# Kernel tuning notes

Measured on AMD Instinct MI355X. Metric: run time of the kernel, lower is better.

The kernel has to match this reference:

```python
import jax, jax.numpy as jnp
import numpy as np

B, F, U, H1, H2 = 2048, 256, 64, 64, 32
E = F + 1  # attention embed dim = num_inputs + 1


def setup_inputs() -> dict:
    key = jax.random.key(0)
    ks = jax.random.split(key, 14)
    s = lambda fan: 1.0 / np.sqrt(fan)
    inp = {
        "x": jax.random.normal(ks[0], (B, F), jnp.float32),
        # stacked per-feature FeatureNN params (Linear(1,U) -> Linear(U,H1) -> Linear(H1,H2) -> Linear(H2,1))
        "w1": jax.random.normal(ks[1], (F, U), jnp.float32) * s(1),
        "b1": jnp.zeros((F, U), jnp.float32),
        "w2": jax.random.normal(ks[2], (F, U, H1), jnp.float32) * s(U),
        "b2": jnp.zeros((F, H1), jnp.float32),
        "w3": jax.random.normal(ks[3], (F, H1, H2), jnp.float32) * s(H1),
        "b3": jnp.zeros((F, H2), jnp.float32),
        "w4": jax.random.normal(ks[4], (F, H2), jnp.float32) * s(H2),
        "b4": jnp.zeros((F,), jnp.float32),
        # MultiheadAttention(E, 1) params: packed qkv in_proj + out_proj
        "in_w": jax.random.normal(ks[5], (3 * E, E), jnp.float32) * s(E),
        "in_b": jnp.zeros((3 * E,), jnp.float32),
        "out_w": jax.random.normal(ks[6], (E, E), jnp.float32) * s(E),
        "out_b": jnp.zeros((E,), jnp.float32),
        "bias": jnp.zeros((1,), jnp.float32),
    }
    return inp


def _attention(x, in_w, in_b, out_w, out_b):
    # x: [B, F]; build [B, F, E] = concat(one-hot feature index, value)
    b = x.shape[0]
    eye = jnp.eye(F, dtype=x.dtype)
    xa = jnp.concatenate([jnp.broadcast_to(eye, (b, F, F)), x[:, :, None]], axis=-1)  # [B,F,E]
    qkv = jnp.einsum("bse,fe->bsf", xa, in_w) + in_b  # [B,F,3E]
    q, k, v = jnp.split(qkv, 3, axis=-1)
    scores = jnp.einsum("bqe,bke->bqk", q, k) / jnp.sqrt(jnp.asarray(E, x.dtype))
    attn = jax.nn.softmax(scores, axis=-1)
    ctx = jnp.einsum("bqk,bke->bqe", attn, v)
    out = jnp.einsum("bqe,fe->bqf", ctx, out_w) + out_b  # out_proj
    return out[:, :, -1]  # keep only the value channel -> [B, F]


def _feature_nns(x, w1, b1, w2, b2, w3, b3, w4, b4):
    # x: [B, F] -> per-feature independent MLPs, batched across features
    h = jax.nn.relu(x[:, :, None] * w1[None] + b1[None])          # [B,F,U]
    h = jax.nn.relu(jnp.einsum("bfu,fuh->bfh", h, w2) + b2[None])  # [B,F,H1]
    h = jax.nn.relu(jnp.einsum("bfh,fhg->bfg", h, w3) + b3[None])  # [B,F,H2]
    return jnp.einsum("bfg,fg->bf", h, w4) + b4[None]              # [B,F]


def reference(x, w1, b1, w2, b2, w3, b3, w4, b4, in_w, in_b, out_w, out_b, bias):
    xa = _attention(x, in_w, in_b, out_w, out_b)                   # att_before_flag=True
    fo = _feature_nns(xa, w1, b1, w2, b2, w3, b3, w4, b4)          # dropout is identity (p=0 / eval)
    out = jnp.sum(fo, axis=-1) + bias                              # [B] + bias -> [B]
    return (out, fo)
```

## Files before the change

### kernel.cpp

```cpp
#include <hip/hip_runtime.h>

#define BB 2048
#define FF 256
#define EE 257
#define UU 64
#define HH1 64
#define HH2 32

#define SC 0.089992807f

typedef __attribute__((ext_vector_type(8))) short short8;
typedef __attribute__((ext_vector_type(4))) float f32x4;
typedef __attribute__((ext_vector_type(4))) unsigned u32x4;
typedef __attribute__((ext_vector_type(2))) unsigned u32x2;

#define MF(a, b, c) __builtin_amdgcn_mfma_f32_16x16x32_bf16(a, b, c, 0, 0, 0)
#define EXP2(x) __builtin_amdgcn_exp2f(x)

__device__ inline unsigned cvt_pk(float a, float b) {
    unsigned r;
    asm("v_cvt_pk_bf16_f32 %0, %1, %2" : "=v"(r) : "v"(a), "v"(b));
    return r;
}
struct HiLo { unsigned hi, lo; };
__device__ inline HiLo split2(float a, float b) {
    HiLo r;
    r.hi = cvt_pk(a, b);
    float ha = __builtin_bit_cast(float, r.hi << 16);
    float hb = __builtin_bit_cast(float, r.hi & 0xFFFF0000u);
    r.lo = cvt_pk(a - ha, b - hb);
    return r;
}
__device__ inline f32x4 splat4(float v) { f32x4 r; r[0]=v; r[1]=v; r[2]=v; r[3]=v; return r; }

__global__ __launch_bounds__(256) void k_prep(const float* __restrict__ in_w,
                                              const float* __restrict__ in_b,
                                              const float* __restrict__ out_w,
                                              const float* __restrict__ out_b,
                                              const float* __restrict__ w2,
                                              const float* __restrict__ w3,
                                              float* __restrict__ mt,
                                              float* __restrict__ uv, float* __restrict__ wgf,
                                              float* __restrict__ sc,
                                              short* __restrict__ w2s, short* __restrict__ w3s) {
    const int blk = blockIdx.x;
    const int t = threadIdx.x;
    __shared__ float red[4][256];
    __shared__ float s0[EE + 3];
    __shared__ float s1[EE + 3];
    if (blk < 256) {
        const int ki = blk;
        for (int j = t; j < EE; j += 256) {
            s0[j] = in_w[(EE + j) * EE + ki] + in_b[EE + j];
            s1[j] = in_b[j];
        }
        __syncthreads();
        const int w = t >> 6, l = t & 63;
        const int j0 = (w * EE) >> 2, j1 = ((w + 1) * EE) >> 2;
        float acc[4] = {0.f, 0.f, 0.f, 0.f};
#pragma unroll 4
        for (int j = j0; j < j1; ++j) {
            float ak = s0[j];
            float bj = s1[j];
#pragma unroll
            for (int g = 0; g < 4; ++g) {
                float aq = in_w[j * EE + l + 64 * g] + bj;
                acc[g] = fmaf(aq, ak, acc[g]);
            }
        }
#pragma unroll
        for (int g = 0; g < 4; ++g) red[w][l + 64 * g] = acc[g];
        __syncthreads();
        {
            float s = red[0][t] + red[1][t] + red[2][t] + red[3][t];
            mt[(ki >> 1) * 512 + t * 2 + (ki & 1)] = s * SC;
        }
    } else if (blk < 512) {
        const int f = blk - 256;
        const int l = t & 63, q = t >> 6;
        const int lr = l & 15, lq = l >> 4;
        const float* w2f = w2 + f * (UU * HH1);
        const float* w3f = w3 + f * (HH1 * HH2);
        short* o2 = w2s + f * 8192;
        short* o3 = w3s + f * 4096;
#pragma unroll
        for (int kb = 0; kb < 2; ++kb) {
            float v[8];
#pragma unroll
            for (int j = 0; j < 8; ++j) v[j] = w2f[(kb * 32 + lq * 8 + j) * HH1 + q * 16 + lr];
            u32x4 hi, lo;
#pragma unroll
            for (int p = 0; p < 4; ++p) {
                HiLo s = split2(v[2 * p], v[2 * p + 1]);
                hi[p] = s.hi; lo[p] = s.lo;
            }
            *(short8*)(o2 + ((0 * 2 + kb) * 4 + q) * 512 + l * 8) = __builtin_bit_cast(short8, hi);
            *(short8*)(o2 + ((1 * 2 + kb) * 4 + q) * 512 + l * 8) = __builtin_bit_cast(short8, lo);
        }
        {
            const int kb = q & 1, ct = q >> 1;
            float v[8];
#pragma unroll
            for (int j = 0; j < 8; ++j) v[j] = w3f[(kb * 32 + lq * 8 + j) * HH2 + ct * 16 + lr];
            u32x4 hi, lo;
#pragma unroll
            for (int p = 0; p < 4; ++p) {
                HiLo s = split2(v[2 * p], v[2 * p + 1]);
                hi[p] = s.hi; lo[p] = s.lo;
            }
            *(short8*)(o3 + ((0 * 2 + kb) * 2 + ct) * 512 + l * 8) = __builtin_bit_cast(short8, hi);
            *(short8*)(o3 + ((1 * 2 + kb) * 2 + ct) * 512 + l * 8) = __builtin_bit_cast(short8, lo);
        }
    } else if (blk < 515) {
        const int which = blk - 512;
        for (int j = t; j < EE; j += 256) {
            if (which == 0)      { s0[j] = in_w[(EE + j) * EE + FF];    s1[j] = in_b[j]; }
            else if (which == 1) { s0[j] = in_w[j * EE + FF];           s1[j] = in_b[EE + j]; }
            else                 { s0[j] = out_w[(EE - 1) * EE + j];    s1[j] = in_b[2 * EE + j]; }
        }
        __syncthreads();
        const int w = t >> 6, l = t & 63;
        const int j0 = (w * EE) >> 2, j1 = ((w + 1) * EE) >> 2;
        const int rowbase = which * EE;
        float acc[4] = {0.f, 0.f, 0.f, 0.f};
#pragma unroll 4
        for (int j = j0; j < j1; ++j) {
            float sk = s0[j];
            float bj = s1[j];
#pragma unroll
            for (int g = 0; g < 4; ++g) {
                float av = in_w[(rowbase + j) * EE + l + 64 * g] + bj;
                acc[g] = fmaf(av, sk, acc[g]);
            }
        }
#pragma unroll
        for (int g = 0; g < 4; ++g) red[w][l + 64 * g] = acc[g];
        __syncthreads();
        {
            float s = red[0][t] + red[1][t] + red[2][t] + red[3][t];
            if (which == 0)      uv[t]          = s * SC;
            else if (which == 1) wgf[2 * t]     = s * SC;
            else                 wgf[2 * t + 1] = s;
        }
    } else {
        const int j = t;
        float cq = in_w[j * EE + FF];
        float ck = in_w[(EE + j) * EE + FF];
        float cv = in_w[(2 * EE + j) * EE + FF];
        float rj = out_w[(EE - 1) * EE + j];
        float pa = cq * ck, pb = cv * rj;
        if (t == 0) {
            const int j2 = 256;
            pa += in_w[j2 * EE + FF] * in_w[(EE + j2) * EE + FF];
            pb += in_w[(2 * EE + j2) * EE + FF] * out_w[(EE - 1) * EE + j2];
        }
#pragma unroll
        for (int o = 32; o > 0; o >>= 1) {
            pa += __shfl_down(pa, o, 64);
            pb += __shfl_down(pb, o, 64);
        }
        if ((t & 63) == 0) { red[0][t >> 6] = pa; red[1][t >> 6] = pb; }
        __syncthreads();
        if (t == 0) {
            pa = red[0][0] + red[0][1] + red[0][2] + red[0][3];
            pb = red[1][0] + red[1][1] + red[1][2] + red[1][3];
            sc[0] = pa * SC;
            sc[1] = pb;
            sc[2] = out_b[EE - 1];
        }
    }
}

__global__ __launch_bounds__(256) void k2_attn(const float* __restrict__ x,
                                               const float2* __restrict__ mt2,
                                               const float* __restrict__ uv,
                                               const float* __restrict__ wg,
                                               const float* __restrict__ sc,
                                               float* __restrict__ xa) {
    const int qi = threadIdx.x;
    const int b0 = blockIdx.x * 2;
    __shared__ __align__(16) float xs0[FF];
    __shared__ __align__(16) float xs1[FF];
    __shared__ __align__(16) float wgs[2 * FF];
    xs0[qi] = x[b0 * FF + qi];
    xs1[qi] = x[(b0 + 1) * FF + qi];
    *(float2*)&wgs[2 * qi] = *(const float2*)&wg[2 * qi];
    const float alpha_s = sc[0], beta = sc[1], ob = sc[2];
    const float uq = uv[qi];
    __syncthreads();
    const float xq0 = xs0[qi];
    const float xq1 = xs1[qi];
    const float a0 = fmaf(alpha_s, xq0, uq);
    const float a1 = fmaf(alpha_s, xq1, uq);
    float le0 = 0.f, le1 = 0.f, p0 = 0.f, p1 = 0.f, q0 = 0.f, q1 = 0.f;
#pragma unroll 8
    for (int kp = 0; kp < FF / 2; ++kp) {
        const float2 m   = mt2[kp * FF + qi];
        const f32x4 wgk  = *(const f32x4*)&wgs[4 * kp];
        const float2 xk0 = *(const float2*)&xs0[2 * kp];
        const float2 xk1 = *(const float2*)&xs1[2 * kp];
        float e;
        e = EXP2(fmaf(xk0.x, a0, fmaf(wgk[0], xq0, m.x))); le0 += e; p0 = fmaf(e, wgk[1], p0); q0 = fmaf(e, xk0.x, q0);
        e = EXP2(fmaf(xk0.y, a0, fmaf(wgk[2], xq0, m.y))); le0 += e; p0 = fmaf(e, wgk[3], p0); q0 = fmaf(e, xk0.y, q0);
        e = EXP2(fmaf(xk1.x, a1, fmaf(wgk[0], xq1, m.x))); le1 += e; p1 = fmaf(e, wgk[1], p1); q1 = fmaf(e, xk1.x, q1);
        e = EXP2(fmaf(xk1.y, a1, fmaf(wgk[2], xq1, m.y))); le1 += e; p1 = fmaf(e, wgk[3], p1); q1 = fmaf(e, xk1.y, q1);
    }
    xa[b0 * FF + qi]       = (p0 + beta * q0) / le0 + ob;
    xa[(b0 + 1) * FF + qi] = (p1 + beta * q1) / le1 + ob;
}

__global__ __launch_bounds__(256, 3) void k3_fnn(const float* xa_in,
                                                 const float* __restrict__ w1,
                                                 const float* __restrict__ b1,
                                                 const float* __restrict__ b2,
                                                 const float* __restrict__ b3,
                                                 const float* __restrict__ w4,
                                                 const float* __restrict__ b4,
                                                 const short* __restrict__ w2s,
                                                 const short* __restrict__ w3s,
                                                 float* fo) {
    const int f   = blockIdx.x & 255;
    const int rq  = blockIdx.x >> 8;
    const int tid = threadIdx.x;
    const int wv  = tid >> 6;
    const int l   = tid & 63;
    const int lr  = l & 15;
    const int lq  = l >> 4;

    const float* w1f = w1 + f * UU;
    const float* b1f = b1 + f * UU;
    const float* b2f = b2 + f * HH1;
    const float* b3f = b3 + f * HH2;
    const float* w4f = w4 + f * HH2;
    const short* w2sf = w2s + f * 8192;
    const short* w3sf = w3s + f * 4096;

    const float B3s0 = b3f[lr], B3s1 = b3f[16 + lr];
    const float w4v0 = w4f[lr], w4v1 = w4f[16 + lr];
    const float b4v  = b4[f];

    short8 W3h[2][2], W3l[2][2];
#pragma unroll
    for (int ct = 0; ct < 2; ++ct)
#pragma unroll
        for (int kb = 0; kb < 2; ++kb) {
            W3h[ct][kb] = *(const short8*)(w3sf + ((0 * 2 + kb) * 2 + ct) * 512 + l * 8);
            W3l[ct][kb] = *(const short8*)(w3sf + ((1 * 2 + kb) * 2 + ct) * 512 + l * 8);
        }

    __shared__ __align__(16) short w2l[8192];
#pragma unroll
    for (int i = 0; i < 4; ++i)
        *(short8*)(w2l + (tid * 4 + i) * 8) = *(const short8*)(w2sf + (tid * 4 + i) * 8);

    __shared__ __align__(16) short lds2[4][32][2][64];
    short* myl = &lds2[wv][0][0][0];

    __syncthreads();

    const int cstart = (rq * 64) / 3;
    const int cend   = ((rq + 1) * 64) / 3;
    for (int ch = cstart + wv; ch < cend; ch += 4) {
        const int rows0 = ch * 32;

        const float xv0 = xa_in[(rows0 + lr) * FF + f];
        const float xv1 = xa_in[(rows0 + 16 + lr) * FF + f];
        short8 Bh[2][2], Bl[2][2];
#pragma unroll
        for (int kb = 0; kb < 2; ++kb) {
            f32x4 wA = *(const f32x4*)(w1f + kb * 32 + lq * 8);
            f32x4 wB = *(const f32x4*)(w1f + kb * 32 + lq * 8 + 4);
            f32x4 bA = *(const f32x4*)(b1f + kb * 32 + lq * 8);
            f32x4 bB = *(const f32x4*)(b1f + kb * 32 + lq * 8 + 4);
#pragma unroll
            for (int rbt = 0; rbt < 2; ++rbt) {
                const float xv = rbt ? xv1 : xv0;
                float h[8];
#pragma unroll
                for (int j = 0; j < 4; ++j) h[j]     = fmaxf(fmaf(xv, wA[j], bA[j]), 0.f);
#pragma unroll
                for (int j = 0; j < 4; ++j) h[4 + j] = fmaxf(fmaf(xv, wB[j], bB[j]), 0.f);
                u32x4 bh, bl;
#pragma unroll
                for (int p = 0; p < 4; ++p) {
                    HiLo s = split2(h[2 * p], h[2 * p + 1]);
                    bh[p] = s.hi; bl[p] = s.lo;
                }
                Bh[rbt][kb] = __builtin_bit_cast(short8, bh);
                Bl[rbt][kb] = __builtin_bit_cast(short8, bl);
            }
        }

#pragma unroll
        for (int ht = 0; ht < 4; ++ht) {
            const short8 W2h0 = *(const short8*)(w2l + (0 * 4 + ht) * 512 + l * 8);
            const short8 W2h1 = *(const short8*)(w2l + (1 * 4 + ht) * 512 + l * 8);
            const short8 W2l0 = *(const short8*)(w2l + (2 * 4 + ht) * 512 + l * 8);
            const short8 W2l1 = *(const short8*)(w2l + (3 * 4 + ht) * 512 + l * 8);
            const f32x4 binit = *(const f32x4*)(b2f + ht * 16 + lq * 4);
#pragma unroll
            for (int rbt = 0; rbt < 2; ++rbt) {
                f32x4 acc = binit;
                acc = MF(W2h0, Bh[rbt][0], acc);
                acc = MF(W2h1, Bh[rbt][1], acc);
                acc = MF(W2h0, Bl[rbt][0], acc);
                acc = MF(W2h1, Bl[rbt][1], acc);
                acc = MF(W2l0, Bh[rbt][0], acc);
                acc = MF(W2l1, Bh[rbt][1], acc);
                const int row = rbt * 16 + lr;
                const int swz = (row & 7) << 3;
                const int hb  = (ht * 16 + lq * 4) ^ swz;
                float v0 = fmaxf(acc[0], 0.f), v1 = fmaxf(acc[1], 0.f);
                float v2 = fmaxf(acc[2], 0.f), v3 = fmaxf(acc[3], 0.f);
                HiLo p0 = split2(v0, v1);
                HiLo p1 = split2(v2, v3);
                u32x2 hiw, low;
                hiw[0] = p0.hi; hiw[1] = p1.hi;
                low[0] = p0.lo; low[1] = p1.lo;
                *(u32x2*)(myl + row * 128 + hb)      = hiw;
                *(u32x2*)(myl + row * 128 + 64 + hb) = low;
            }
        }

#pragma unroll
        for (int rbt = 0; rbt < 2; ++rbt) {
            const int row = rbt * 16 + lr;
            const int swz = (row & 7) << 3;
            const short8 Ah0 = *(const short8*)(myl + row * 128 + ((0  + lq * 8) ^ swz));
            const short8 Ah1 = *(const short8*)(myl + row * 128 + ((32 + lq * 8) ^ swz));
            const short8 Al0 = *(const short8*)(myl + row * 128 + 64 + ((0  + lq * 8) ^ swz));
            const short8 Al1 = *(const short8*)(myl + row * 128 + 64 + ((32 + lq * 8) ^ swz));
            f32x4 a0 = splat4(B3s0);
            f32x4 a1 = splat4(B3s1);
            a0 = MF(Ah0, W3h[0][0], a0); a0 = MF(Ah1, W3h[0][1], a0);
            a0 = MF(Ah0, W3l[0][0], a0); a0 = MF(Ah1, W3l[0][1], a0);
            a0 = MF(Al0, W3h[0][0], a0); a0 = MF(Al1, W3h[0][1], a0);
            a1 = MF(Ah0, W3h[1][0], a1); a1 = MF(Ah1, W3h[1][1], a1);
            a1 = MF(Ah0, W3l[1][0], a1); a1 = MF(Ah1, W3l[1][1], a1);
            a1 = MF(Al0, W3h[1][0], a1); a1 = MF(Al1, W3h[1][1], a1);
            float sr0 = fmaf(fmaxf(a0[0], 0.f), w4v0, fmaxf(a1[0], 0.f) * w4v1);
            float sr1 = fmaf(fmaxf(a0[1], 0.f), w4v0, fmaxf(a1[1], 0.f) * w4v1);
            float sr2 = fmaf(fmaxf(a0[2], 0.f), w4v0, fmaxf(a1[2], 0.f) * w4v1);
            float sr3 = fmaf(fmaxf(a0[3], 0.f), w4v0, fmaxf(a1[3], 0.f) * w4v1);
#pragma unroll
            for (int m = 1; m < 16; m <<= 1) {
                sr0 += __shfl_xor(sr0, m, 64);
                sr1 += __shfl_xor(sr1, m, 64);
                sr2 += __shfl_xor(sr2, m, 64);
                sr3 += __shfl_xor(sr3, m, 64);
            }
            if (lr == 0) {
                const int rb = rows0 + rbt * 16 + lq * 4;
                fo[(rb + 0) * FF + f] = sr0 + b4v;
                fo[(rb + 1) * FF + f] = sr1 + b4v;
                fo[(rb + 2) * FF + f] = sr2 + b4v;
                fo[(rb + 3) * FF + f] = sr3 + b4v;
            }
        }
    }
}

__global__ __launch_bounds__(64) void k4_sum(const float* __restrict__ fo,
                                             const float* __restrict__ bias,
                                             float* __restrict__ out) {
    const int b = blockIdx.x;
    const int t = threadIdx.x;
    const float* r = fo + b * FF;
    float s = r[t] + r[t + 64] + r[t + 128] + r[t + 192];
#pragma unroll
    for (int o = 32; o > 0; o >>= 1) s += __shfl_down(s, o, 64);
    if (t == 0) out[b] = s + bias[0];
}

extern "C" void kernel_launch(void* const* d_in, const int* in_sizes, int n_in,
                              void* d_out, int out_size, void* d_ws, size_t ws_size,
                              hipStream_t stream) {
    const float* x    = (const float*)d_in[0];
    const float* w1   = (const float*)d_in[1];
    const float* b1   = (const float*)d_in[2];
    const float* w2   = (const float*)d_in[3];
    const float* b2   = (const float*)d_in[4];
    const float* w3   = (const float*)d_in[5];
    const float* b3   = (const float*)d_in[6];
    const float* w4   = (const float*)d_in[7];
    const float* b4   = (const float*)d_in[8];
    const float* in_w = (const float*)d_in[9];
    const float* in_b = (const float*)d_in[10];
    const float* out_w= (const float*)d_in[11];
    const float* out_b= (const float*)d_in[12];
    const float* bias = (const float*)d_in[13];

    float* out = (float*)d_out;
    float* fo  = out + BB;
    float* ws  = (float*)d_ws;
    float* mt  = ws;
    float* uvp = ws + 65536;
    float* wgp = ws + 65792;
    float* scp = ws + 66304;
    short* w2s = (short*)(ws + 66560);
    short* w3s = w2s + 256 * 8192;

    k_prep<<<516, 256, 0, stream>>>(in_w, in_b, out_w, out_b, w2, w3,
                                    mt, uvp, wgp, scp, w2s, w3s);
    k2_attn<<<BB / 2, 256, 0, stream>>>(x, (const float2*)mt, uvp, wgp, scp, fo);
    k3_fnn<<<FF * 3, 256, 0, stream>>>(fo, w1, b1, b2, b3, w4, b4, w2s, w3s, fo);
    k4_sum<<<BB, 64, 0, stream>>>(fo, bias, out);
}
```

Before: 73.96 us.

## Keep layer-2 MFMA outputs in registers via permuted W2 layout, skip LDS round-trip

```diff
diff --git a/kernel.cpp b/kernel.cpp
--- a/kernel.cpp
+++ b/kernel.cpp
@@ -31,7 +31,6 @@
     r.lo = cvt_pk(a - ha, b - hb);
     return r;
 }
-__device__ inline f32x4 splat4(float v) { f32x4 r; r[0]=v; r[1]=v; r[2]=v; r[3]=v; return r; }
 
 __global__ __launch_bounds__(256) void k_prep(const float* __restrict__ in_w,
                                               const float* __restrict__ in_b,
@@ -83,11 +82,12 @@
         const float* w3f = w3 + f * (HH1 * HH2);
         short* o2 = w2s + f * 8192;
         short* o3 = w3s + f * 4096;
+        const int hperm = (q & 1) * 32 + (lr >> 2) * 8 + ((q >> 1) << 2) + (lr & 3);
 #pragma unroll
         for (int kb = 0; kb < 2; ++kb) {
             float v[8];
 #pragma unroll
-            for (int j = 0; j < 8; ++j) v[j] = w2f[(kb * 32 + lq * 8 + j) * HH1 + q * 16 + lr];
+            for (int j = 0; j < 8; ++j) v[j] = w2f[(kb * 32 + lq * 8 + j) * HH1 + hperm];
             u32x4 hi, lo;
 #pragma unroll
             for (int p = 0; p < 4; ++p) {
@@ -219,7 +219,8 @@
                                                  const short* __restrict__ w2s,
                                                  const short* __restrict__ w3s,
                                                  float* fo) {
-    const int f   = blockIdx.x & 255;
+    const int fidx = blockIdx.x & 255;
+    const int f   = ((fidx & 7) << 5) | (fidx >> 3);
     const int rq  = blockIdx.x >> 8;
     const int tid = threadIdx.x;
     const int wv  = tid >> 6;
@@ -234,9 +235,6 @@
     const float* w4f = w4 + f * HH2;
     const short* w2sf = w2s + f * 8192;
     const short* w3sf = w3s + f * 4096;
-
-    const float B3s0 = b3f[lr], B3s1 = b3f[16 + lr];
-    const float w4v0 = w4f[lr], w4v1 = w4f[16 + lr];
     const float b4v  = b4[f];
 
     short8 W3h[2][2], W3l[2][2];
@@ -247,24 +245,33 @@
             W3h[ct][kb] = *(const short8*)(w3sf + ((0 * 2 + kb) * 2 + ct) * 512 + l * 8);
             W3l[ct][kb] = *(const short8*)(w3sf + ((1 * 2 + kb) * 2 + ct) * 512 + l * 8);
         }
+    f32x4 B3v[2], W4v[2];
+#pragma unroll
+    for (int ct = 0; ct < 2; ++ct) {
+        B3v[ct] = *(const f32x4*)(b3f + ct * 16 + lq * 4);
+        W4v[ct] = *(const f32x4*)(w4f + ct * 16 + lq * 4);
+    }
 
     __shared__ __align__(16) short w2l[8192];
 #pragma unroll
     for (int i = 0; i < 4; ++i)
         *(short8*)(w2l + (tid * 4 + i) * 8) = *(const short8*)(w2sf + (tid * 4 + i) * 8);
-
-    __shared__ __align__(16) short lds2[4][32][2][64];
-    short* myl = &lds2[wv][0][0][0];
-
     __syncthreads();
 
     const int cstart = (rq * 64) / 3;
     const int cend   = ((rq + 1) * 64) / 3;
-    for (int ch = cstart + wv; ch < cend; ch += 4) {
+    int ch = cstart + wv;
+    if (ch >= cend) return;
+    float xv0 = xa_in[(ch * 32 + lr) * FF + f];
+    float xv1 = xa_in[(ch * 32 + 16 + lr) * FF + f];
+    for (; ch < cend; ch += 4) {
         const int rows0 = ch * 32;
-
-        const float xv0 = xa_in[(rows0 + lr) * FF + f];
-        const float xv1 = xa_in[(rows0 + 16 + lr) * FF + f];
+        float nxv0 = 0.f, nxv1 = 0.f;
+        if (ch + 4 < cend) {
+            nxv0 = xa_in[((ch + 4) * 32 + lr) * FF + f];
+            nxv1 = xa_in[((ch + 4) * 32 + 16 + lr) * FF + f];
+        }
+
         short8 Bh[2][2], Bl[2][2];
 #pragma unroll
         for (int kb = 0; kb < 2; ++kb) {
@@ -291,72 +298,65 @@
             }
         }
 
+        f32x4 acc[2][4];
 #pragma unroll
         for (int ht = 0; ht < 4; ++ht) {
             const short8 W2h0 = *(const short8*)(w2l + (0 * 4 + ht) * 512 + l * 8);
             const short8 W2h1 = *(const short8*)(w2l + (1 * 4 + ht) * 512 + l * 8);
             const short8 W2l0 = *(const short8*)(w2l + (2 * 4 + ht) * 512 + l * 8);
             const short8 W2l1 = *(const short8*)(w2l + (3 * 4 + ht) * 512 + l * 8);
-            const f32x4 binit = *(const f32x4*)(b2f + ht * 16 + lq * 4);
+            const f32x4 binit = *(const f32x4*)(b2f + (ht & 1) * 32 + lq * 8 + ((ht >> 1) << 2));
 #pragma unroll
             for (int rbt = 0; rbt < 2; ++rbt) {
-                f32x4 acc = binit;
-                acc = MF(W2h0, Bh[rbt][0], acc);
-                acc = MF(W2h1, Bh[rbt][1], acc);
-                acc = MF(W2h0, Bl[rbt][0], acc);
-                acc = MF(W2h1, Bl[rbt][1], acc);
-                acc = MF(W2l0, Bh[rbt][0], acc);
-                acc = MF(W2l1, Bh[rbt][1], acc);
-                const int row = rbt * 16 + lr;
-                const int swz = (row & 7) << 3;
-                const int hb  = (ht * 16 + lq * 4) ^ swz;
-                float v0 = fmaxf(acc[0], 0.f), v1 = fmaxf(acc[1], 0.f);
-                float v2 = fmaxf(acc[2], 0.f), v3 = fmaxf(acc[3], 0.f);
-                HiLo p0 = split2(v0, v1);
-                HiLo p1 = split2(v2, v3);
-                u32x2 hiw, low;
-                hiw[0] = p0.hi; hiw[1] = p1.hi;
-                low[0] = p0.lo; low[1] = p1.lo;
-                *(u32x2*)(myl + row * 128 + hb)      = hiw;
-                *(u32x2*)(myl + row * 128 + 64 + hb) = low;
+                f32x4 a = binit;
+                a = MF(W2h0, Bh[rbt][0], a);
+                a = MF(W2h1, Bh[rbt][1], a);
+                a = MF(W2h0, Bl[rbt][0], a);
+                a = MF(W2h1, Bl[rbt][1], a);
+                a = MF(W2l0, Bh[rbt][0], a);
+                a = MF(W2l1, Bh[rbt][1], a);
+                acc[rbt][ht] = a;
             }
         }
 
 #pragma unroll
         for (int rbt = 0; rbt < 2; ++rbt) {
-            const int row = rbt * 16 + lr;
-            const int swz = (row & 7) << 3;
-            const short8 Ah0 = *(const short8*)(myl + row * 128 + ((0  + lq * 8) ^ swz));
-            const short8 Ah1 = *(const short8*)(myl + row * 128 + ((32 + lq * 8) ^ swz));
-            const short8 Al0 = *(const short8*)(myl + row * 128 + 64 + ((0  + lq * 8) ^ swz));
-            const short8 Al1 = *(const short8*)(myl + row * 128 + 64 + ((32 + lq * 8) ^ swz));
-            f32x4 a0 = splat4(B3s0);
-            f32x4 a1 = splat4(B3s1);
-            a0 = MF(Ah0, W3h[0][0], a0); a0 = MF(Ah1, W3h[0][1], a0);
-            a0 = MF(Ah0, W3l[0][0], a0); a0 = MF(Ah1, W3l[0][1], a0);
-            a0 = MF(Al0, W3h[0][0], a0); a0 = MF(Al1, W3h[0][1], a0);
-            a1 = MF(Ah0, W3h[1][0], a1); a1 = MF(Ah1, W3h[1][1], a1);
-            a1 = MF(Ah0, W3l[1][0], a1); a1 = MF(Ah1, W3l[1][1], a1);
-            a1 = MF(Al0, W3h[1][0], a1); a1 = MF(Al1, W3h[1][1], a1);
-            float sr0 = fmaf(fmaxf(a0[0], 0.f), w4v0, fmaxf(a1[0], 0.f) * w4v1);
-            float sr1 = fmaf(fmaxf(a0[1], 0.f), w4v0, fmaxf(a1[1], 0.f) * w4v1);
-            float sr2 = fmaf(fmaxf(a0[2], 0.f), w4v0, fmaxf(a1[2], 0.f) * w4v1);
-            float sr3 = fmaf(fmaxf(a0[3], 0.f), w4v0, fmaxf(a1[3], 0.f) * w4v1);
-#pragma unroll
-            for (int m = 1; m < 16; m <<= 1) {
-                sr0 += __shfl_xor(sr0, m, 64);
-                sr1 += __shfl_xor(sr1, m, 64);
-                sr2 += __shfl_xor(sr2, m, 64);
-                sr3 += __shfl_xor(sr3, m, 64);
-            }
-            if (lr == 0) {
-                const int rb = rows0 + rbt * 16 + lq * 4;
-                fo[(rb + 0) * FF + f] = sr0 + b4v;
-                fo[(rb + 1) * FF + f] = sr1 + b4v;
-                fo[(rb + 2) * FF + f] = sr2 + b4v;
-                fo[(rb + 3) * FF + f] = sr3 + b4v;
-            }
-        }
+            short8 Bh3[2], Bl3[2];
+#pragma unroll
+            for (int kb = 0; kb < 2; ++kb) {
+                float e0 = fmaxf(acc[rbt][kb][0], 0.f),     e1 = fmaxf(acc[rbt][kb][1], 0.f);
+                float e2 = fmaxf(acc[rbt][kb][2], 0.f),     e3 = fmaxf(acc[rbt][kb][3], 0.f);
+                float e4 = fmaxf(acc[rbt][kb + 2][0], 0.f), e5 = fmaxf(acc[rbt][kb + 2][1], 0.f);
+                float e6 = fmaxf(acc[rbt][kb + 2][2], 0.f), e7 = fmaxf(acc[rbt][kb + 2][3], 0.f);
+                HiLo p0 = split2(e0, e1), p1 = split2(e2, e3);
+                HiLo p2 = split2(e4, e5), p3 = split2(e6, e7);
+                u32x4 bh, bl;
+                bh[0] = p0.hi; bh[1] = p1.hi; bh[2] = p2.hi; bh[3] = p3.hi;
+                bl[0] = p0.lo; bl[1] = p1.lo; bl[2] = p2.lo; bl[3] = p3.lo;
+                Bh3[kb] = __builtin_bit_cast(short8, bh);
+                Bl3[kb] = __builtin_bit_cast(short8, bl);
+            }
+            float part = 0.f;
+#pragma unroll
+            for (int ct = 0; ct < 2; ++ct) {
+                f32x4 a2 = B3v[ct];
+                a2 = MF(W3h[ct][0], Bh3[0], a2);
+                a2 = MF(W3h[ct][1], Bh3[1], a2);
+                a2 = MF(W3h[ct][0], Bl3[0], a2);
+                a2 = MF(W3h[ct][1], Bl3[1], a2);
+                a2 = MF(W3l[ct][0], Bh3[0], a2);
+                a2 = MF(W3l[ct][1], Bh3[1], a2);
+#pragma unroll
+                for (int r = 0; r < 4; ++r)
+                    part = fmaf(fmaxf(a2[r], 0.f), W4v[ct][r], part);
+            }
+            part += __shfl_xor(part, 16, 64);
+            part += __shfl_xor(part, 32, 64);
+            if (lq == 0)
+                fo[(rows0 + rbt * 16 + lr) * FF + f] = part + b4v;
+        }
+
+        xv0 = nxv0; xv1 = nxv1;
     }
 }
 
```

Measured after the change: 66.73 us. 1.11x faster.
